# Optimization experiments

Measured on AMD Instinct MI355X. Metric: run time of the kernel, lower is better.

Reference implementation:

```python
import jax, jax.numpy as jnp
import numpy as np

B, H, L, D = 2, 16, 2048, 64


def setup_inputs() -> dict:
    key = jax.random.key(0)
    kq, kk, kv = jax.random.split(key, 3)
    return {
        "query": jax.random.normal(kq, (B, H, L, D), dtype=jnp.float32),
        "key": jax.random.normal(kk, (B, H, L, D), dtype=jnp.float32),
        "value": jax.random.normal(kv, (B, H, L, D), dtype=jnp.float32),
        "dhead": D,
        "causal": 1,
    }


def reference(query, key, value, dhead, causal):
    # mode='dhead': muP attention with scale 1/dhead (not 1/sqrt(dhead)).
    # Inputs/outputs in [B, H, L, D] layout (the torch code transposes to
    # [B, L, H, D] for the einsum and transposes back; net layout is the same).
    scale = 1.0 / dhead
    a = jnp.einsum('bhld,bhLd->bhlL', query, key) * scale  # [B,H,L,L]
    if causal:
        seq = a.shape[-1]
        mask = jnp.tril(jnp.ones((seq, seq), dtype=bool))  # [L,L]
        a = jnp.where(mask, a, jnp.float32(-jnp.inf))
    a = jax.nn.softmax(a, axis=-1)
    out = jnp.einsum('bhlL,bhLd->bhld', a, value)  # [B,H,L,D]
    return out
```

## Files before the change

### kernel.cpp

```cpp
#include <hip/hip_runtime.h>

#define BHH 32
#define SEQ 2048
#define DH 64
#define BK 64
#define NKT (SEQ / BK)
#define NT  (BHH * NKT)

typedef __attribute__((ext_vector_type(8))) _Float16 half8_t;
typedef __attribute__((ext_vector_type(4))) _Float16 half4_t;
typedef __attribute__((ext_vector_type(2))) _Float16 half2_t;
typedef __attribute__((ext_vector_type(16))) float f32x16;

__device__ __forceinline__ void async_copy16(const void* g, const void* lds) {
    __builtin_amdgcn_global_load_lds(
        (const __attribute__((address_space(1))) unsigned int*)g,
        (__attribute__((address_space(3))) unsigned int*)lds, 16, 0, 0);
}

__device__ __forceinline__ half2_t pkrtz(float a, float b) {
    return __builtin_bit_cast(half2_t, __builtin_amdgcn_cvt_pkrtz(a, b));
}

__device__ __forceinline__ half8_t cat8(half2_t a, half2_t b, half2_t c, half2_t d) {
    half4_t lo = __builtin_shufflevector(a, b, 0, 1, 2, 3);
    half4_t hi = __builtin_shufflevector(c, d, 0, 1, 2, 3);
    return __builtin_shufflevector(lo, hi, 0, 1, 2, 3, 4, 5, 6, 7);
}

__global__ __launch_bounds__(256) void prep_kv(const float* __restrict__ K,
                                               const float* __restrict__ V,
                                               _Float16* __restrict__ Kf,
                                               _Float16* __restrict__ Vf) {
    __shared__ _Float16 l[64 * 76];
    const int t = threadIdx.x;
    const int wave = t >> 6, lane = t & 63, l31 = lane & 31, h = lane >> 5;
    const int row = t >> 2, col0 = (t & 3) * 16;
    int b = blockIdx.x;

    if (b < NT) {
        const float4* src = (const float4*)(K + (size_t)b * 4096 + row * 64 + col0);
        #pragma unroll
        for (int q = 0; q < 2; ++q) {
            float4 f0 = src[q * 2], f1 = src[q * 2 + 1];
            half8_t w = { (_Float16)f0.x, (_Float16)f0.y, (_Float16)f0.z, (_Float16)f0.w,
                          (_Float16)f1.x, (_Float16)f1.y, (_Float16)f1.z, (_Float16)f1.w };
            *(half8_t*)&l[row * 72 + col0 + q * 8] = w;
        }
        __syncthreads();
        #pragma unroll
        for (int p = 0; p < 2; ++p) {
            const int frag = wave * 2 + p, kb = frag >> 2, tt = frag & 3;
            half8_t w = *(const half8_t*)&l[(kb * 32 + l31) * 72 + tt * 16 + h * 8];
            *(half8_t*)&Kf[(size_t)b * 4096 + frag * 512 + lane * 8] = w;
        }
    } else {
        b -= NT;
        const float4* src = (const float4*)(V + (size_t)b * 4096 + row * 64 + col0);
        #pragma unroll
        for (int q = 0; q < 4; ++q) {
            float4 f = src[q];
            half4_t w = { (_Float16)f.x, (_Float16)f.y, (_Float16)f.z, (_Float16)f.w };
            *(half4_t*)&l[row * 76 + col0 + q * 4] = w;
        }
        __syncthreads();
        #pragma unroll
        for (int p = 0; p < 2; ++p) {
            const int frag = wave * 2 + p, dn = frag >> 2, s = frag & 3;
            const int bb = s >> 1, tt = s & 1;
            half8_t w;
            #pragma unroll
            for (int j = 0; j < 8; ++j) {
                const int krow = bb * 32 + tt * 16 + (j & 3) + (j >> 2) * 8 + h * 4;
                w[j] = l[krow * 76 + dn * 32 + l31];
            }
            *(half8_t*)&Vf[(size_t)b * 4096 + frag * 512 + lane * 8] = w;
        }
    }
}

__global__ __launch_bounds__(256, 2) void fattn_kernel(
        const float* __restrict__ Q, const _Float16* __restrict__ Kf,
        const _Float16* __restrict__ Vf, float* __restrict__ O) {
    const int bh = blockIdx.x & 31;
    const int G  = blockIdx.x >> 5;
    const int qb = (G < 4) ? 15 - G : (G < 8) ? 11 - G + 0
                 : (G < 12) ? G : G - 12;
    const int nkt = 2 * qb + 2;
    const int ktdiag = 2 * qb;
    const int tid  = threadIdx.x;
    const int wave = tid >> 6;
    const int lane = tid & 63;
    const int l31  = lane & 31;
    const int h    = lane >> 5;

    __shared__ _Float16 ldsK[2][4096];
    __shared__ _Float16 ldsV[2][4096];

    const size_t base = (size_t)bh * SEQ * DH;
    const int qrow  = qb * 128 + wave * 32;
    const int q_abs = qrow + l31;
    const size_t tb = (size_t)(bh * NKT) * 4096;

    const _Float16* gsrc = ((wave < 2) ? Kf : Vf) + tb + (wave & 1) * 2048 + lane * 8;
    _Float16* dst0 = ((wave < 2) ? &ldsK[0][0] : &ldsV[0][0]) + (wave & 1) * 2048;
    _Float16* dst1 = ((wave < 2) ? &ldsK[1][0] : &ldsV[1][0]) + (wave & 1) * 2048;

    #define STAGE(kt_, dd_) do {                                         \
        const _Float16* s_ = gsrc + (size_t)(kt_) * 4096;                \
        _Float16* d_ = (dd_);                                            \
        async_copy16(s_,        d_);                                     \
        async_copy16(s_ + 512,  d_ + 512);                               \
        async_copy16(s_ + 1024, d_ + 1024);                              \
        async_copy16(s_ + 1536, d_ + 1536);                              \
    } while (0)

    STAGE(0, dst0);

    const float qscale = 1.44269504f / 64.0f;
    half8_t qf[4];
    {
        const float* qp = Q + base + (size_t)q_abs * DH + h * 8;
        #pragma unroll
        for (int t = 0; t < 4; ++t) {
            float4 a = *(const float4*)(qp + t * 16);
            float4 b2 = *(const float4*)(qp + t * 16 + 4);
            qf[t] = (half8_t){
                (_Float16)(a.x * qscale), (_Float16)(a.y * qscale),
                (_Float16)(a.z * qscale), (_Float16)(a.w * qscale),
                (_Float16)(b2.x * qscale), (_Float16)(b2.y * qscale),
                (_Float16)(b2.z * qscale), (_Float16)(b2.w * qscale) };
        }
    }
    asm volatile("s_waitcnt vmcnt(0) lgkmcnt(0)\n\ts_barrier" ::: "memory");

    f32x16 acc0 = {}, acc1 = {};
    float l_lane = 0.f;

    const _Float16* kbase = &ldsK[0][0] + lane * 8;
    const _Float16* vbase = &ldsV[0][0] + lane * 8;

    for (int kt = 0; kt < nkt; ++kt) {
        const _Float16* kk = kbase + (kt & 1) * 4096;
        const _Float16* vv = vbase + (kt & 1) * 4096;
        if (kt + 1 < nkt) STAGE(kt + 1, ((kt + 1) & 1) ? dst1 : dst0);

        half8_t kreg[8], vreg[8];
        #pragma unroll
        for (int f = 0; f < 8; ++f) kreg[f] = *(const half8_t*)(kk + f * 512);
        #pragma unroll
        for (int f = 0; f < 8; ++f) vreg[f] = *(const half8_t*)(vv + f * 512);
        asm volatile("" ::: "memory");

        f32x16 st0 = {}, st1 = {};
        st0 = __builtin_amdgcn_mfma_f32_32x32x16_f16(kreg[0], qf[0], st0, 0, 0, 0);
        st0 = __builtin_amdgcn_mfma_f32_32x32x16_f16(kreg[1], qf[1], st0, 0, 0, 0);
        st0 = __builtin_amdgcn_mfma_f32_32x32x16_f16(kreg[2], qf[2], st0, 0, 0, 0);
        st0 = __builtin_amdgcn_mfma_f32_32x32x16_f16(kreg[3], qf[3], st0, 0, 0, 0);
        st1 = __builtin_amdgcn_mfma_f32_32x32x16_f16(kreg[4], qf[0], st1, 0, 0, 0);
        st1 = __builtin_amdgcn_mfma_f32_32x32x16_f16(kreg[5], qf[1], st1, 0, 0, 0);
        st1 = __builtin_amdgcn_mfma_f32_32x32x16_f16(kreg[6], qf[2], st1, 0, 0, 0);
        st1 = __builtin_amdgcn_mfma_f32_32x32x16_f16(kreg[7], qf[3], st1, 0, 0, 0);

        float p0[16], p1[16];
        #pragma unroll
        for (int r = 0; r < 16; ++r) {
            p0[r] = __builtin_amdgcn_exp2f(st0[r]);
            p1[r] = __builtin_amdgcn_exp2f(st1[r]);
        }

        if (kt >= ktdiag) {
            const int kb0 = kt * 64 + h * 4;
            #pragma unroll
            for (int r = 0; r < 16; ++r) {
                const int ka = kb0 + (r & 3) + (r >> 2) * 8;
                if (ka > q_abs)      p0[r] = 0.f;
                if (ka + 32 > q_abs) p1[r] = 0.f;
            }
        }

        {
            float a0 = (p0[0] + p0[1]) + (p0[2] + p0[3]);
            float a1 = (p0[4] + p0[5]) + (p0[6] + p0[7]);
            float a2 = (p0[8] + p0[9]) + (p0[10] + p0[11]);
            float a3 = (p0[12] + p0[13]) + (p0[14] + p0[15]);
            float b0 = (p1[0] + p1[1]) + (p1[2] + p1[3]);
            float b1 = (p1[4] + p1[5]) + (p1[6] + p1[7]);
            float b2 = (p1[8] + p1[9]) + (p1[10] + p1[11]);
            float b3 = (p1[12] + p1[13]) + (p1[14] + p1[15]);
            l_lane += ((a0 + a1) + (a2 + a3)) + ((b0 + b1) + (b2 + b3));
        }

        half8_t pb00 = cat8(pkrtz(p0[0], p0[1]),  pkrtz(p0[2], p0[3]),
                            pkrtz(p0[4], p0[5]),  pkrtz(p0[6], p0[7]));
        half8_t pb01 = cat8(pkrtz(p0[8], p0[9]),  pkrtz(p0[10], p0[11]),
                            pkrtz(p0[12], p0[13]), pkrtz(p0[14], p0[15]));
        half8_t pb10 = cat8(pkrtz(p1[0], p1[1]),  pkrtz(p1[2], p1[3]),
                            pkrtz(p1[4], p1[5]),  pkrtz(p1[6], p1[7]));
        half8_t pb11 = cat8(pkrtz(p1[8], p1[9]),  pkrtz(p1[10], p1[11]),
                            pkrtz(p1[12], p1[13]), pkrtz(p1[14], p1[15]));

        acc0 = __builtin_amdgcn_mfma_f32_32x32x16_f16(vreg[0], pb00, acc0, 0, 0, 0);
        acc0 = __builtin_amdgcn_mfma_f32_32x32x16_f16(vreg[1], pb01, acc0, 0, 0, 0);
        acc0 = __builtin_amdgcn_mfma_f32_32x32x16_f16(vreg[2], pb10, acc0, 0, 0, 0);
        acc0 = __builtin_amdgcn_mfma_f32_32x32x16_f16(vreg[3], pb11, acc0, 0, 0, 0);
        acc1 = __builtin_amdgcn_mfma_f32_32x32x16_f16(vreg[4], pb00, acc1, 0, 0, 0);
        acc1 = __builtin_amdgcn_mfma_f32_32x32x16_f16(vreg[5], pb01, acc1, 0, 0, 0);
        acc1 = __builtin_amdgcn_mfma_f32_32x32x16_f16(vreg[6], pb10, acc1, 0, 0, 0);
        acc1 = __builtin_amdgcn_mfma_f32_32x32x16_f16(vreg[7], pb11, acc1, 0, 0, 0);

        asm volatile("s_waitcnt vmcnt(0) lgkmcnt(0)\n\ts_barrier" ::: "memory");
    }

    {
        float l_i = l_lane + __shfl_xor(l_lane, 32);
        const float rl = 1.0f / l_i;
        float* op = O + base + (size_t)q_abs * DH + h * 4;
        #pragma unroll
        for (int g4 = 0; g4 < 4; ++g4) {
            float4 o0;
            o0.x = acc0[g4 * 4 + 0] * rl;
            o0.y = acc0[g4 * 4 + 1] * rl;
            o0.z = acc0[g4 * 4 + 2] * rl;
            o0.w = acc0[g4 * 4 + 3] * rl;
            *(float4*)(op + g4 * 8) = o0;
            float4 o1;
            o1.x = acc1[g4 * 4 + 0] * rl;
            o1.y = acc1[g4 * 4 + 1] * rl;
            o1.z = acc1[g4 * 4 + 2] * rl;
            o1.w = acc1[g4 * 4 + 3] * rl;
            *(float4*)(op + 32 + g4 * 8) = o1;
        }
    }
    #undef STAGE
}

extern "C" void kernel_launch(void* const* d_in, const int* in_sizes, int n_in,
                              void* d_out, int out_size, void* d_ws, size_t ws_size,
                              hipStream_t stream) {
    const float* Q = (const float*)d_in[0];
    const float* K = (const float*)d_in[1];
    const float* V = (const float*)d_in[2];
    float* O = (float*)d_out;
    _Float16* Kf = (_Float16*)d_ws;
    _Float16* Vf = Kf + (size_t)NT * 4096;
    prep_kv<<<2 * NT, 256, 0, stream>>>(K, V, Kf, Vf);
    fattn_kernel<<<16 * BHH, 256, 0, stream>>>(Q, Kf, Vf, O);
}
```

Baseline: 125.5 us.

## Use single-wave blocks reading K/V tiles directly from global memory

Splits each 128-row query block into four independent single-wave workgroups of 32 query rows and drops the LDS double-buffered async staging and block barriers. Each wave loads its K/V fragments directly from global memory, relying on L2/L1 for reuse across waves sharing a head. The per-wave causal loop length becomes finer-grained, removing barrier and LDS costs at the price of more global/cache traffic and no explicit prefetch overlap.

```diff
diff --git a/kernel.cpp b/kernel.cpp
--- a/kernel.cpp
+++ b/kernel.cpp
@@ -11,12 +11,6 @@
 typedef __attribute__((ext_vector_type(4))) _Float16 half4_t;
 typedef __attribute__((ext_vector_type(2))) _Float16 half2_t;
 typedef __attribute__((ext_vector_type(16))) float f32x16;
-
-__device__ __forceinline__ void async_copy16(const void* g, const void* lds) {
-    __builtin_amdgcn_global_load_lds(
-        (const __attribute__((address_space(1))) unsigned int*)g,
-        (__attribute__((address_space(3))) unsigned int*)lds, 16, 0, 0);
-}
 
 __device__ __forceinline__ half2_t pkrtz(float a, float b) {
     return __builtin_bit_cast(half2_t, __builtin_amdgcn_cvt_pkrtz(a, b));
@@ -79,43 +73,23 @@
     }
 }
 
-__global__ __launch_bounds__(256, 2) void fattn_kernel(
+__global__ __launch_bounds__(64, 2) void fattn_kernel(
         const float* __restrict__ Q, const _Float16* __restrict__ Kf,
         const _Float16* __restrict__ Vf, float* __restrict__ O) {
-    const int bh = blockIdx.x & 31;
-    const int G  = blockIdx.x >> 5;
-    const int qb = (G < 4) ? 15 - G : (G < 8) ? 11 - G + 0
-                 : (G < 12) ? G : G - 12;
-    const int nkt = 2 * qb + 2;
-    const int ktdiag = 2 * qb;
-    const int tid  = threadIdx.x;
-    const int wave = tid >> 6;
-    const int lane = tid & 63;
+    const int bh  = blockIdx.x & 31;
+    const int q32 = 63 - (blockIdx.x >> 5);
+    const int ktd = q32 >> 1;
+    const int nkt = ktd + 1;
+    const int lane = threadIdx.x;
     const int l31  = lane & 31;
     const int h    = lane >> 5;
 
-    __shared__ _Float16 ldsK[2][4096];
-    __shared__ _Float16 ldsV[2][4096];
-
     const size_t base = (size_t)bh * SEQ * DH;
-    const int qrow  = qb * 128 + wave * 32;
-    const int q_abs = qrow + l31;
+    const int q_abs = q32 * 32 + l31;
     const size_t tb = (size_t)(bh * NKT) * 4096;
 
-    const _Float16* gsrc = ((wave < 2) ? Kf : Vf) + tb + (wave & 1) * 2048 + lane * 8;
-    _Float16* dst0 = ((wave < 2) ? &ldsK[0][0] : &ldsV[0][0]) + (wave & 1) * 2048;
-    _Float16* dst1 = ((wave < 2) ? &ldsK[1][0] : &ldsV[1][0]) + (wave & 1) * 2048;
-
-    #define STAGE(kt_, dd_) do {                                         \
-        const _Float16* s_ = gsrc + (size_t)(kt_) * 4096;                \
-        _Float16* d_ = (dd_);                                            \
-        async_copy16(s_,        d_);                                     \
-        async_copy16(s_ + 512,  d_ + 512);                               \
-        async_copy16(s_ + 1024, d_ + 1024);                              \
-        async_copy16(s_ + 1536, d_ + 1536);                              \
-    } while (0)
-
-    STAGE(0, dst0);
+    const _Float16* kp = Kf + tb + lane * 8;
+    const _Float16* vp = Vf + tb + lane * 8;
 
     const float qscale = 1.44269504f / 64.0f;
     half8_t qf[4];
@@ -132,25 +106,19 @@
                 (_Float16)(b2.z * qscale), (_Float16)(b2.w * qscale) };
         }
     }
-    asm volatile("s_waitcnt vmcnt(0) lgkmcnt(0)\n\ts_barrier" ::: "memory");
 
     f32x16 acc0 = {}, acc1 = {};
     float l_lane = 0.f;
 
-    const _Float16* kbase = &ldsK[0][0] + lane * 8;
-    const _Float16* vbase = &ldsV[0][0] + lane * 8;
-
     for (int kt = 0; kt < nkt; ++kt) {
-        const _Float16* kk = kbase + (kt & 1) * 4096;
-        const _Float16* vv = vbase + (kt & 1) * 4096;
-        if (kt + 1 < nkt) STAGE(kt + 1, ((kt + 1) & 1) ? dst1 : dst0);
+        const _Float16* kk = kp + (size_t)kt * 4096;
+        const _Float16* vv = vp + (size_t)kt * 4096;
 
         half8_t kreg[8], vreg[8];
         #pragma unroll
         for (int f = 0; f < 8; ++f) kreg[f] = *(const half8_t*)(kk + f * 512);
         #pragma unroll
         for (int f = 0; f < 8; ++f) vreg[f] = *(const half8_t*)(vv + f * 512);
-        asm volatile("" ::: "memory");
 
         f32x16 st0 = {}, st1 = {};
         st0 = __builtin_amdgcn_mfma_f32_32x32x16_f16(kreg[0], qf[0], st0, 0, 0, 0);
@@ -169,7 +137,7 @@
             p1[r] = __builtin_amdgcn_exp2f(st1[r]);
         }
 
-        if (kt >= ktdiag) {
+        if (kt == ktd) {
             const int kb0 = kt * 64 + h * 4;
             #pragma unroll
             for (int r = 0; r < 16; ++r) {
@@ -208,8 +176,6 @@
         acc1 = __builtin_amdgcn_mfma_f32_32x32x16_f16(vreg[5], pb01, acc1, 0, 0, 0);
         acc1 = __builtin_amdgcn_mfma_f32_32x32x16_f16(vreg[6], pb10, acc1, 0, 0, 0);
         acc1 = __builtin_amdgcn_mfma_f32_32x32x16_f16(vreg[7], pb11, acc1, 0, 0, 0);
-
-        asm volatile("s_waitcnt vmcnt(0) lgkmcnt(0)\n\ts_barrier" ::: "memory");
     }
 
     {
@@ -232,7 +198,6 @@
             *(float4*)(op + 32 + g4 * 8) = o1;
         }
     }
-    #undef STAGE
 }
 
 extern "C" void kernel_launch(void* const* d_in, const int* in_sizes, int n_in,
@@ -245,5 +210,5 @@
     _Float16* Kf = (_Float16*)d_ws;
     _Float16* Vf = Kf + (size_t)NT * 4096;
     prep_kv<<<2 * NT, 256, 0, stream>>>(K, V, Kf, Vf);
-    fattn_kernel<<<16 * BHH, 256, 0, stream>>>(Q, Kf, Vf, O);
-}
+    fattn_kernel<<<64 * BHH, 64, 0, stream>>>(Q, Kf, Vf, O);
+}
```

Result: slower. 139.8 us (+11.4%).
